# Optimization experiments

Measured on AMD Instinct MI355X. Metric: run time of the kernel, lower is better.

## Reference

```python
import jax, jax.numpy as jnp
import numpy as np

B, T, S, U = 64, 64, 128, 4  # batch, frames, yt_img_size, upscale_factor
P, U2 = S * S, U * U          # per-pixel batch dim, tiny-matmul output dim
RECON = S * U                 # 512


def setup_inputs() -> dict:
    key = jax.random.key(0)
    k1, k2, k3 = jax.random.split(key, 3)
    yt = jax.random.normal(k1, (B, T, S, S), dtype=jnp.float32)
    weights = jax.random.normal(k2, (P, T, U2), dtype=jnp.float32)
    biases = jax.random.normal(k3, (P, 1, U2), dtype=jnp.float32)
    return {"yt": yt, "weights": weights, "biases": biases}


def reference(yt, weights, biases):
    # (B, T, S, S) -> (P, B, T): one tiny (B,T)x(T,U2) GEMM per pixel location
    y = yt.reshape(B, T, P).transpose(2, 0, 1)
    # per-location batched matmul + bias: (P, B, U2)
    up = jnp.einsum('pbt,ptu->pbu', y, weights) + biases
    # pixel-shuffle style upsampling: (S, S, B, U, U) -> (B, S, U, S, U) -> (B, 1, 512, 512)
    up = up.reshape(S, S, B, U, U).transpose(2, 0, 3, 1, 4)
    out = up.reshape(B, RECON, RECON)[:, None, :, :]
    # seq_block is identity in this configuration
    return out
```

## Files before the change

### kernel.cpp

```cpp
#include <hip/hip_runtime.h>

namespace {
constexpr int Sdim = 128;
constexpr int Tdim = 64;
constexpr int U2c  = 16;
constexpr int PT   = 32;
constexpr int NTHREADS = 256;
constexpr int PP = Sdim * Sdim;
constexpr int TQ = 16;
constexpr int NSTG = Tdim / TQ;
}

__global__ __launch_bounds__(NTHREADS, 2)
void upscale_fused(const float* __restrict__ yt,
                   const float* __restrict__ wgt,
                   const float* __restrict__ bias,
                   float* __restrict__ out)
{
    __shared__ float wlds[TQ * U2c * PT];

    const int tid   = threadIdx.x;
    const int p_blk = blockIdx.x * PT;

    const int pg = tid & 15;
    const int bq = tid >> 4;
    const int p0 = p_blk + pg * 2;

    const float4* wgt4 = reinterpret_cast<const float4*>(wgt);

    auto stage = [&](int stg) {
        #pragma unroll
        for (int i = 0; i < 8; ++i) {
            const int f = i * NTHREADS + tid;
            const int r = f >> 6;
            const int c = f & 63;
            const float4 v = wgt4[(size_t)(p_blk + r) * 256 + (size_t)stg * 64 + c];
            const int tw = c >> 2;
            const int uq = c & 3;
            const int col = r ^ (2 * tw);
            float* dst = &wlds[(tw * U2c + uq * 4) * PT + col];
            dst[0 * PT] = v.x;  dst[1 * PT] = v.y;
            dst[2 * PT] = v.z;  dst[3 * PT] = v.w;
        }
    };

    stage(0);

    float acc[4][2][16];
    #pragma unroll
    for (int jp = 0; jp < 2; ++jp) {
        const float* bp = bias + (size_t)(p0 + jp) * U2c;
        #pragma unroll
        for (int q = 0; q < 4; ++q) {
            const float4 v = *reinterpret_cast<const float4*>(bp + q * 4);
            #pragma unroll
            for (int k = 0; k < 4; ++k) {
                acc[k][jp][q * 4 + 0] = v.x;  acc[k][jp][q * 4 + 1] = v.y;
                acc[k][jp][q * 4 + 2] = v.z;  acc[k][jp][q * 4 + 3] = v.w;
            }
        }
    }

    const float* ybase = yt + (size_t)bq * ((size_t)Tdim * PP) + p0;
    auto ldy = [&](int t, float2* dst) {
        #pragma unroll
        for (int k = 0; k < 4; ++k)
            dst[k] = *reinterpret_cast<const float2*>(
                ybase + (size_t)k * 16 * Tdim * PP + (size_t)t * PP);
    };

    auto step = [&](const float2* y, int tl) {
        const float* wrow = &wlds[tl * (U2c * PT) + ((pg * 2) ^ (2 * tl))];
        #pragma unroll
        for (int u = 0; u < 16; ++u) {
            const float2 wv = *reinterpret_cast<const float2*>(wrow + u * PT);
            #pragma unroll
            for (int k = 0; k < 4; ++k) {
                acc[k][0][u] = fmaf(y[k].x, wv.x, acc[k][0][u]);
                acc[k][1][u] = fmaf(y[k].y, wv.y, acc[k][1][u]);
            }
        }
    };

    float2 yc[4], yn[4];
    ldy(0, yc);
    ldy(1, yn);

    __syncthreads();

    #pragma unroll 1
    for (int stg = 0; stg < NSTG; ++stg) {
        #pragma unroll 1
        for (int tq = 0; tq < TQ; tq += 2) {
            const int tg = stg * TQ + tq;
            step(yc, tq);
            if (tg + 2 < Tdim) ldy(tg + 2, yc);
            step(yn, tq + 1);
            if (tg + 3 < Tdim) ldy(tg + 3, yn);
        }
        if (stg + 1 < NSTG) {
            __syncthreads();
            stage(stg + 1);
            __syncthreads();
        }
    }

    const int s1   = p_blk / Sdim;
    const int s2_0 = p_blk % Sdim;

    #pragma unroll
    for (int k = 0; k < 4; ++k) {
        const int b = bq + 16 * k;
        float* ob = out + (size_t)b * (512 * 512);
        #pragma unroll
        for (int jp = 0; jp < 2; ++jp) {
            const int c0 = (s2_0 + pg * 2 + jp) * 4;
            #pragma unroll
            for (int u1 = 0; u1 < 4; ++u1) {
                const int r = s1 * 4 + u1;
                float4 v;
                v.x = acc[k][jp][u1 * 4 + 0];
                v.y = acc[k][jp][u1 * 4 + 1];
                v.z = acc[k][jp][u1 * 4 + 2];
                v.w = acc[k][jp][u1 * 4 + 3];
                *reinterpret_cast<float4*>(ob + (size_t)r * 512 + c0) = v;
            }
        }
    }
}

extern "C" void kernel_launch(void* const* d_in, const int* in_sizes, int n_in,
                              void* d_out, int out_size, void* d_ws, size_t ws_size,
                              hipStream_t stream)
{
    const float* yt   = (const float*)d_in[0];
    const float* wgt  = (const float*)d_in[1];
    const float* bias = (const float*)d_in[2];
    float* outp       = (float*)d_out;

    dim3 grid(PP / PT);
    dim3 block(NTHREADS);
    hipLaunchKernelGGL(upscale_fused, grid, block, 0, stream, yt, wgt, bias, outp);
}
```

Baseline: 107.3 us.

## Double-buffer weight LDS stages and widen pixel tile to 64 per block

Weight slices are now staged into two LDS buffers, so the next stage loads while the current one is computed, leaving one barrier per stage instead of two. The block grows to 512 threads covering 64 pixels, each thread doing 4 pixels by 2 batches with float4 loads of yt and of weights from LDS. The t-chunk per stage shrinks to 8. This aims to hide weight-load latency and widen the vector memory accesses, at the cost of a larger block and a changed register and occupancy balance under launch_bounds(512, 2).

```diff
diff --git a/kernel.cpp b/kernel.cpp
--- a/kernel.cpp
+++ b/kernel.cpp
@@ -4,10 +4,10 @@
 constexpr int Sdim = 128;
 constexpr int Tdim = 64;
 constexpr int U2c  = 16;
-constexpr int PT   = 32;
-constexpr int NTHREADS = 256;
+constexpr int PT   = 64;
+constexpr int NTHREADS = 512;
 constexpr int PP = Sdim * Sdim;
-constexpr int TQ = 16;
+constexpr int TQ = 8;
 constexpr int NSTG = Tdim / TQ;
 }
 
@@ -17,72 +17,73 @@
                    const float* __restrict__ bias,
                    float* __restrict__ out)
 {
-    __shared__ float wlds[TQ * U2c * PT];
+    __shared__ float wlds[2][TQ * U2c * PT];
 
     const int tid   = threadIdx.x;
     const int p_blk = blockIdx.x * PT;
 
     const int pg = tid & 15;
-    const int bq = tid >> 4;
-    const int p0 = p_blk + pg * 2;
+    const int b2 = tid >> 4;
+    const int p0 = p_blk + pg * 4;
 
     const float4* wgt4 = reinterpret_cast<const float4*>(wgt);
 
-    auto stage = [&](int stg) {
+    auto stage = [&](int stg, int buf) {
         #pragma unroll
-        for (int i = 0; i < 8; ++i) {
+        for (int i = 0; i < 4; ++i) {
             const int f = i * NTHREADS + tid;
-            const int r = f >> 6;
-            const int c = f & 63;
-            const float4 v = wgt4[(size_t)(p_blk + r) * 256 + (size_t)stg * 64 + c];
-            const int tw = c >> 2;
+            const int r = f >> 5;
+            const int c = f & 31;
+            const float4 v = wgt4[(size_t)(p_blk + r) * 256 + (size_t)stg * 32 + c];
+            const int tl = c >> 2;
             const int uq = c & 3;
-            const int col = r ^ (2 * tw);
-            float* dst = &wlds[(tw * U2c + uq * 4) * PT + col];
+            const int col = r ^ (4 * tl);
+            float* dst = &wlds[buf][(tl * U2c + uq * 4) * PT + col];
             dst[0 * PT] = v.x;  dst[1 * PT] = v.y;
             dst[2 * PT] = v.z;  dst[3 * PT] = v.w;
         }
     };
 
-    stage(0);
+    stage(0, 0);
 
-    float acc[4][2][16];
+    float acc[2][4][16];
     #pragma unroll
-    for (int jp = 0; jp < 2; ++jp) {
-        const float* bp = bias + (size_t)(p0 + jp) * U2c;
+    for (int j = 0; j < 4; ++j) {
+        const float* bp = bias + (size_t)(p0 + j) * U2c;
         #pragma unroll
         for (int q = 0; q < 4; ++q) {
             const float4 v = *reinterpret_cast<const float4*>(bp + q * 4);
-            #pragma unroll
-            for (int k = 0; k < 4; ++k) {
-                acc[k][jp][q * 4 + 0] = v.x;  acc[k][jp][q * 4 + 1] = v.y;
-                acc[k][jp][q * 4 + 2] = v.z;  acc[k][jp][q * 4 + 3] = v.w;
-            }
+            acc[0][j][q * 4 + 0] = v.x;  acc[0][j][q * 4 + 1] = v.y;
+            acc[0][j][q * 4 + 2] = v.z;  acc[0][j][q * 4 + 3] = v.w;
+            acc[1][j][q * 4 + 0] = v.x;  acc[1][j][q * 4 + 1] = v.y;
+            acc[1][j][q * 4 + 2] = v.z;  acc[1][j][q * 4 + 3] = v.w;
         }
     }
 
-    const float* ybase = yt + (size_t)bq * ((size_t)Tdim * PP) + p0;
-    auto ldy = [&](int t, float2* dst) {
-        #pragma unroll
-        for (int k = 0; k < 4; ++k)
-            dst[k] = *reinterpret_cast<const float2*>(
-                ybase + (size_t)k * 16 * Tdim * PP + (size_t)t * PP);
+    const float* y0b = yt + (size_t)b2 * ((size_t)Tdim * PP) + p0;
+    const float* y1b = y0b + (size_t)32 * Tdim * PP;
+    float4 yc[2], yn[2];
+    auto ldy = [&](int t, float4* dst) {
+        dst[0] = *reinterpret_cast<const float4*>(y0b + (size_t)t * PP);
+        dst[1] = *reinterpret_cast<const float4*>(y1b + (size_t)t * PP);
     };
 
-    auto step = [&](const float2* y, int tl) {
-        const float* wrow = &wlds[tl * (U2c * PT) + ((pg * 2) ^ (2 * tl))];
+    auto step = [&](const float4* y, int tl, int buf) {
+        const float* base = &wlds[buf][tl * (U2c * PT) + ((pg * 4) ^ (4 * tl))];
         #pragma unroll
         for (int u = 0; u < 16; ++u) {
-            const float2 wv = *reinterpret_cast<const float2*>(wrow + u * PT);
-            #pragma unroll
-            for (int k = 0; k < 4; ++k) {
-                acc[k][0][u] = fmaf(y[k].x, wv.x, acc[k][0][u]);
-                acc[k][1][u] = fmaf(y[k].y, wv.y, acc[k][1][u]);
-            }
+            const float4 wv = *reinterpret_cast<const float4*>(base + u * PT);
+            acc[0][0][u] = fmaf(y[0].x, wv.x, acc[0][0][u]);
+            acc[0][1][u] = fmaf(y[0].y, wv.y, acc[0][1][u]);
+            acc[0][2][u] = fmaf(y[0].z, wv.z, acc[0][2][u]);
+            acc[0][3][u] = fmaf(y[0].w, wv.w, acc[0][3][u]);
+            acc[1][0][u] = fmaf(y[1].x, wv.x, acc[1][0][u]);
+            acc[1][1][u] = fmaf(y[1].y, wv.y, acc[1][1][u]);
+            acc[1][2][u] = fmaf(y[1].z, wv.z, acc[1][2][u]);
+            acc[1][3][u] = fmaf(y[1].w, wv.w, acc[1][3][u]);
         }
     };
 
-    float2 yc[4], yn[4];
     ldy(0, yc);
     ldy(1, yn);
 
@@ -90,39 +91,38 @@
 
     #pragma unroll 1
     for (int stg = 0; stg < NSTG; ++stg) {
+        const int buf = stg & 1;
+        if (stg + 1 < NSTG) stage(stg + 1, buf ^ 1);
+
         #pragma unroll 1
         for (int tq = 0; tq < TQ; tq += 2) {
             const int tg = stg * TQ + tq;
-            step(yc, tq);
+            step(yc, tq, buf);
             if (tg + 2 < Tdim) ldy(tg + 2, yc);
-            step(yn, tq + 1);
+            step(yn, tq + 1, buf);
             if (tg + 3 < Tdim) ldy(tg + 3, yn);
         }
-        if (stg + 1 < NSTG) {
-            __syncthreads();
-            stage(stg + 1);
-            __syncthreads();
-        }
+        if (stg + 1 < NSTG) __syncthreads();
     }
 
     const int s1   = p_blk / Sdim;
     const int s2_0 = p_blk % Sdim;
 
     #pragma unroll
-    for (int k = 0; k < 4; ++k) {
-        const int b = bq + 16 * k;
+    for (int bi = 0; bi < 2; ++bi) {
+        const int b = b2 + bi * 32;
         float* ob = out + (size_t)b * (512 * 512);
         #pragma unroll
-        for (int jp = 0; jp < 2; ++jp) {
-            const int c0 = (s2_0 + pg * 2 + jp) * 4;
+        for (int j = 0; j < 4; ++j) {
+            const int c0 = (s2_0 + pg * 4 + j) * 4;
             #pragma unroll
             for (int u1 = 0; u1 < 4; ++u1) {
                 const int r = s1 * 4 + u1;
                 float4 v;
-                v.x = acc[k][jp][u1 * 4 + 0];
-                v.y = acc[k][jp][u1 * 4 + 1];
-                v.z = acc[k][jp][u1 * 4 + 2];
-                v.w = acc[k][jp][u1 * 4 + 3];
+                v.x = acc[bi][j][u1 * 4 + 0];
+                v.y = acc[bi][j][u1 * 4 + 1];
+                v.z = acc[bi][j][u1 * 4 + 2];
+                v.w = acc[bi][j][u1 * 4 + 3];
                 *reinterpret_cast<float4*>(ob + (size_t)r * 512 + c0) = v;
             }
         }
```

Result: slower. 357.8 us (+233.5%).
